# Kernel tuning notes

Hardware: AMD Instinct MI355X
Metric: run time of the kernel (lower is better)

Reference implementation:

```python
import jax, jax.numpy as jnp
import numpy as np

NUM_GRAPHS = 256
NEG_SLOPE = 0.2


def gat_layer(x, src, dst, W, a_src, a_dst, bias, concat):
    # x: [N, Fin], W: [Fin, H*C], a_src/a_dst: [H, C], bias: [H*C] or [C]
    N = x.shape[0]
    H, C = a_src.shape
    xl = (x @ W).reshape(N, H, C)                      # per-head projections
    e_src = jnp.sum(xl * a_src, axis=-1)               # [N, H]
    e_dst = jnp.sum(xl * a_dst, axis=-1)               # [N, H]
    e = jax.nn.leaky_relu(e_src[src] + e_dst[dst], NEG_SLOPE)  # [E, H]
    # edge softmax over variable-size neighbor sets (grouped by dst)
    m = jax.ops.segment_max(e, dst, num_segments=N)    # [N, H]
    m = jnp.where(jnp.isfinite(m), m, 0.0)
    ee = jnp.exp(e - m[dst])
    s = jax.ops.segment_sum(ee, dst, num_segments=N)   # [N, H]
    alpha = ee / (s[dst] + 1e-16)                      # [E, H]
    msg = alpha[:, :, None] * xl[src]                  # [E, H, C]
    out = jax.ops.segment_sum(msg, dst, num_segments=N)  # [N, H, C]
    out = out.reshape(N, H * C) if concat else out.mean(axis=1)
    return out + bias


def setup_inputs() -> dict:
    key = jax.random.key(0)
    ks = jax.random.split(key, 12)
    N, E, Fin, H, C, Fout = 100000, 1600000, 128, 8, 16, 64
    x = jax.random.normal(ks[0], (N, Fin), dtype=jnp.float32)
    edge_index = jax.random.randint(ks[1], (2, E), 0, N, dtype=jnp.int32)
    batch = jnp.sort(jax.random.randint(ks[2], (N,), 0, NUM_GRAPHS, dtype=jnp.int32))
    sc = 0.1
    W1 = jax.random.normal(ks[3], (Fin, H * C), dtype=jnp.float32) * sc
    att_src1 = jax.random.normal(ks[4], (H, C), dtype=jnp.float32) * sc
    att_dst1 = jax.random.normal(ks[5], (H, C), dtype=jnp.float32) * sc
    bias1 = jnp.zeros((H * C,), dtype=jnp.float32)
    W2 = jax.random.normal(ks[6], (H * C, Fout), dtype=jnp.float32) * sc
    att_src2 = jax.random.normal(ks[7], (1, Fout), dtype=jnp.float32) * sc
    att_dst2 = jax.random.normal(ks[8], (1, Fout), dtype=jnp.float32) * sc
    bias2 = jnp.zeros((Fout,), dtype=jnp.float32)
    return {"x": x, "W1": W1, "att_src1": att_src1, "att_dst1": att_dst1,
            "bias1": bias1, "W2": W2, "att_src2": att_src2, "att_dst2": att_dst2,
            "bias2": bias2, "edge_index": edge_index, "batch": batch}


def reference(x, W1, att_src1, att_dst1, bias1, W2, att_src2, att_dst2, bias2,
              edge_index, batch):
    N = x.shape[0]
    loop = jnp.arange(N, dtype=edge_index.dtype)
    src = jnp.concatenate([edge_index[0], loop])  # add self-loops (PyG default)
    dst = jnp.concatenate([edge_index[1], loop])
    # dropout is identity in eval mode
    h = gat_layer(x, src, dst, W1, att_src1, att_dst1, bias1, concat=True)
    h = jax.nn.elu(h)
    h = gat_layer(h, src, dst, W2, att_src2, att_dst2, bias2, concat=False)
    # global mean pooling over graphs
    sums = jax.ops.segment_sum(h, batch, num_segments=NUM_GRAPHS)
    cnts = jax.ops.segment_sum(jnp.ones((N,), h.dtype), batch, num_segments=NUM_GRAPHS)
    return sums / jnp.maximum(cnts, 1.0)[:, None]
```

## Files before the change

### kernel.cpp

```cpp
#include <hip/hip_runtime.h>
#include <hip/hip_fp16.h>


#define LRELU_SLOPE 0.2f
#define NBLKB 512
#define NBUCK 256
#define LOG2E 1.4426950408889634f

__device__ __forceinline__ float lrelu(float x) { return x > 0.f ? x : LRELU_SLOPE * x; }

typedef _Float16 f16x8 __attribute__((ext_vector_type(8)));
typedef float f32x4 __attribute__((ext_vector_type(4)));

template<typename TX, int M_, int HEADS>
__global__ __launch_bounds__(256) void gemm_mfma(const TX* __restrict__ X,
    const __half* __restrict__ Wt, __half* __restrict__ Y,
    const float* __restrict__ as, const float* __restrict__ ad,
    float* __restrict__ es, float* __restrict__ ed, int N) {
  constexpr int K = 128;
  constexpr int BM = 64;
  constexpr int LP = K + 8;
  __shared__ _Float16 Xl[BM * LP];
  const int tid = threadIdx.x;
  const int row0 = blockIdx.x * BM;

  if constexpr (sizeof(TX) == 4) {
    for (int i = tid; i < BM * (K / 4); i += 256) {
      const int r = i / (K / 4), c4 = (i % (K / 4)) * 4;
      int gr = row0 + r; if (gr >= N) gr = N - 1;
      const float4 v = *(const float4*)((const float*)X + (size_t)gr * K + c4);
      _Float16* d = &Xl[r * LP + c4];
      d[0] = (_Float16)v.x; d[1] = (_Float16)v.y;
      d[2] = (_Float16)v.z; d[3] = (_Float16)v.w;
    }
  } else {
    for (int i = tid; i < BM * (K / 8); i += 256) {
      const int r = i / (K / 8), c8 = (i % (K / 8)) * 8;
      int gr = row0 + r; if (gr >= N) gr = N - 1;
      const f16x8 v = *(const f16x8*)((const _Float16*)X + (size_t)gr * K + c8);
      *(f16x8*)&Xl[r * LP + c8] = v;
    }
  }
  __syncthreads();

  const int w = tid >> 6, l = tid & 63;
  const int lrow = l & 15, lk = (l >> 4) * 8;
  constexpr int NT = M_ / 16;
  f32x4 acc[NT];
#pragma unroll
  for (int n = 0; n < NT; ++n) acc[n] = (f32x4){0.f, 0.f, 0.f, 0.f};

#pragma unroll
  for (int kk = 0; kk < K; kk += 32) {
    const f16x8 a = *(const f16x8*)&Xl[(w * 16 + lrow) * LP + kk + lk];
#pragma unroll
    for (int n = 0; n < NT; ++n) {
      const f16x8 b = *(const f16x8*)((const _Float16*)Wt +
                        (size_t)(n * 16 + lrow) * K + kk + lk);
      acc[n] = __builtin_amdgcn_mfma_f32_16x16x32_f16(a, b, acc[n], 0, 0, 0);
    }
  }
  const int orow = row0 + w * 16 + (l >> 4) * 4;
#pragma unroll
  for (int n = 0; n < NT; ++n) {
#pragma unroll
    for (int j = 0; j < 4; ++j) {
      const int gr = orow + j;
      if (gr < N) Y[(size_t)gr * M_ + n * 16 + lrow] = __float2half(acc[n][j]);
    }
  }

  if constexpr (HEADS == 8) {
#pragma unroll
    for (int n = 0; n < NT; ++n) {
#pragma unroll
      for (int j = 0; j < 4; ++j) {
        float ps = acc[n][j] * as[n * 16 + lrow];
        float pd = acc[n][j] * ad[n * 16 + lrow];
#pragma unroll
        for (int o = 1; o <= 8; o <<= 1) {
          ps += __shfl_xor(ps, o);
          pd += __shfl_xor(pd, o);
        }
        if (lrow == n) {
          const int gr = orow + j;
          if (gr < N) { es[gr * 8 + n] = ps * LOG2E; ed[gr * 8 + n] = pd * LOG2E; }
        }
      }
    }
  } else {
#pragma unroll
    for (int j = 0; j < 4; ++j) {
      float ps = 0.f, pd = 0.f;
#pragma unroll
      for (int n = 0; n < NT; ++n) {
        ps += acc[n][j] * as[n * 16 + lrow];
        pd += acc[n][j] * ad[n * 16 + lrow];
      }
#pragma unroll
      for (int o = 1; o <= 8; o <<= 1) {
        ps += __shfl_xor(ps, o);
        pd += __shfl_xor(pd, o);
      }
      if (lrow == 0) {
        const int gr = orow + j;
        if (gr < N) { es[gr] = ps * LOG2E; ed[gr] = pd * LOG2E; }
      }
    }
  }
}

__global__ __launch_bounds__(1024) void hist_conv(const int* __restrict__ ei, int E,
    int* __restrict__ bh, const float* __restrict__ W1, const float* __restrict__ W2,
    __half* __restrict__ Wt1, __half* __restrict__ Wt2) {
  const int t = threadIdx.x;
  if (blockIdx.x < NBLKB) {
    __shared__ int hist[NBUCK];
    if (t < NBUCK) hist[t] = 0;
    __syncthreads();
    const int chunk = (E + NBLKB - 1) / NBLKB;
    const int s0 = blockIdx.x * chunk;
    const int s1 = min(E, s0 + chunk);
    for (int e = s0 + t; e < s1; e += 1024) atomicAdd(&hist[ei[E + e] >> 9], 1);
    __syncthreads();
    if (t < NBUCK) bh[t * NBLKB + blockIdx.x] = hist[t];
  } else {
    const int i = (blockIdx.x - NBLKB) * 1024 + t;
    if (i < 128 * 128) {
      const int k = i >> 7, m = i & 127;
      Wt1[m * 128 + k] = __float2half(W1[i]);
    } else if (i < 128 * 128 + 128 * 64) {
      const int j = i - 128 * 128;
      const int k = j >> 6, m = j & 63;
      Wt2[m * 128 + k] = __float2half(W2[j]);
    }
  }
}

__global__ __launch_bounds__(256) void scanA(int* __restrict__ a, int* __restrict__ ctot, int N) {
  __shared__ int sm[256];
  const int base = blockIdx.x * 1024;
  const int t = threadIdx.x;
  int v[4], s = 0;
#pragma unroll
  for (int i = 0; i < 4; ++i) {
    const int idx = base + t * 4 + i;
    v[i] = (idx < N) ? a[idx] : 0;
    s += v[i];
  }
  sm[t] = s;
  __syncthreads();
  for (int o = 1; o < 256; o <<= 1) {
    const int x = (t >= o) ? sm[t - o] : 0;
    __syncthreads();
    sm[t] += x;
    __syncthreads();
  }
  if (t == 255) ctot[blockIdx.x] = sm[255];
  int run = sm[t] - s;
#pragma unroll
  for (int i = 0; i < 4; ++i) {
    const int idx = base + t * 4 + i;
    if (idx < N) a[idx] = run;
    run += v[i];
  }
}

__global__ __launch_bounds__(256) void scanC(int* __restrict__ a,
    const int* __restrict__ ctot, int NCH, int Ntot) {
  __shared__ int sc[128];
  const int t = threadIdx.x;
  if (t < 128) sc[t] = (t < NCH) ? ctot[t] : 0;
  __syncthreads();
  for (int o = 1; o < 128; o <<= 1) {
    int x = 0;
    if (t < 128 && t >= o) x = sc[t - o];
    __syncthreads();
    if (t < 128) sc[t] += x;
    __syncthreads();
  }
  const int i = blockIdx.x * 256 + t;
  if (i < Ntot) {
    const int c = i >> 10;
    a[i] += (c == 0) ? 0 : sc[c - 1];
  }
}

__global__ __launch_bounds__(1024) void bucket_scatter(const int* __restrict__ ei, int E,
    const int* __restrict__ bh, int* __restrict__ eb) {
  __shared__ int offs[NBUCK];
  const int t = threadIdx.x;
  if (t < NBUCK) offs[t] = bh[t * NBLKB + blockIdx.x];
  __syncthreads();
  const int chunk = (E + NBLKB - 1) / NBLKB;
  const int s0 = blockIdx.x * chunk;
  const int s1 = min(E, s0 + chunk);
  for (int e = s0 + t; e < s1; e += 1024) {
    const int s = ei[e], d = ei[E + e];
    const int pos = atomicAdd(&offs[d >> 9], 1);
    eb[pos] = (s << 9) | (d & 511);
  }
}

__global__ __launch_bounds__(512) void csr_bucket(const int* __restrict__ eb,
    const int* __restrict__ bh, int E, int N,
    int* __restrict__ rowptr, int* __restrict__ csr) {
  __shared__ int deg[512];
  __shared__ int sm[512];
  const int t = threadIdx.x;
  const int bucket = blockIdx.x;
  const int bstart = bh[bucket * NBLKB];
  const int bend = (bucket + 1 < NBUCK) ? bh[(bucket + 1) * NBLKB] : E;
  const int n0 = bucket << 9;
  deg[t] = 0;
  __syncthreads();
  for (int j = bstart + t; j < bend; j += 512) atomicAdd(&deg[eb[j] & 511], 1);
  __syncthreads();
  const int v = deg[t];
  sm[t] = v;
  __syncthreads();
  for (int o = 1; o < 512; o <<= 1) {
    const int x = (t >= o) ? sm[t - o] : 0;
    __syncthreads();
    sm[t] += x;
    __syncthreads();
  }
  if (n0 + t < N) rowptr[n0 + t] = bstart + sm[t];
  deg[t] = bstart + sm[t] - v;
  __syncthreads();
  const int nband = (N + 8191) >> 13;
  for (int b = 0; b < nband; ++b) {
    for (int j = bstart + t; j < bend; j += 512) {
      const int e = eb[j];
      if ((e >> 22) == b) {
        const int pos = atomicAdd(&deg[e & 511], 1);
        csr[pos] = e >> 9;
      }
    }
  }
}

__global__ __launch_bounds__(256) void gather_h8(const __half* __restrict__ xl,
    const float* __restrict__ es, const float* __restrict__ ed,
    const int* __restrict__ rowptr, const int* __restrict__ csr,
    const float* __restrict__ bias, __half* __restrict__ hout, int N) {
  const int wave = threadIdx.x >> 6, lane = threadIdx.x & 63;
  const int n = blockIdx.x * 4 + wave;
  if (n >= N) return;
  const int sub = lane >> 5;
  const int sl  = lane & 31;
  const int c0  = sl * 4;
  const int h   = sl >> 2;
  const float edv = ed[n * 8 + h];
  const int start = (n == 0) ? 0 : rowptr[n - 1];
  const int end   = rowptr[n];
  union U8 { uint2 u; __half2 h2[2]; };

  float4 acc = make_float4(0.f, 0.f, 0.f, 0.f);
  float ssum = 0.f;
  if (sub == 0) {
    const float ee = exp2f(lrelu(es[n * 8 + h] + edv));
    U8 r; r.u = *(const uint2*)&xl[(size_t)n * 128 + c0];
    const float2 f0 = __half22float2(r.h2[0]), f1 = __half22float2(r.h2[1]);
    acc.x = ee * f0.x; acc.y = ee * f0.y; acc.z = ee * f1.x; acc.w = ee * f1.y;
    ssum = ee;
  }
  int j = start + sub;
  for (; j + 6 < end; j += 8) {
    int s0 = csr[j], s1 = csr[j + 2], s2 = csr[j + 4], s3 = csr[j + 6];
    float ev[4]; U8 r[4];
    ev[0] = es[s0 * 8 + h]; r[0].u = *(const uint2*)&xl[(size_t)s0 * 128 + c0];
    ev[1] = es[s1 * 8 + h]; r[1].u = *(const uint2*)&xl[(size_t)s1 * 128 + c0];
    ev[2] = es[s2 * 8 + h]; r[2].u = *(const uint2*)&xl[(size_t)s2 * 128 + c0];
    ev[3] = es[s3 * 8 + h]; r[3].u = *(const uint2*)&xl[(size_t)s3 * 128 + c0];
#pragma unroll
    for (int k = 0; k < 4; ++k) {
      const float ee = exp2f(lrelu(ev[k] + edv));
      const float2 f0 = __half22float2(r[k].h2[0]), f1 = __half22float2(r[k].h2[1]);
      acc.x += ee * f0.x; acc.y += ee * f0.y;
      acc.z += ee * f1.x; acc.w += ee * f1.y;
      ssum += ee;
    }
  }
  for (; j < end; j += 2) {
    const int src = csr[j];
    const float ee = exp2f(lrelu(es[src * 8 + h] + edv));
    U8 r; r.u = *(const uint2*)&xl[(size_t)src * 128 + c0];
    const float2 f0 = __half22float2(r.h2[0]), f1 = __half22float2(r.h2[1]);
    acc.x += ee * f0.x; acc.y += ee * f0.y;
    acc.z += ee * f1.x; acc.w += ee * f1.y;
    ssum += ee;
  }
  acc.x += __shfl_xor(acc.x, 32); acc.y += __shfl_xor(acc.y, 32);
  acc.z += __shfl_xor(acc.z, 32); acc.w += __shfl_xor(acc.w, 32);
  ssum  += __shfl_xor(ssum, 32);
  if (sub == 0) {
    const float inv = 1.f / (ssum + 1e-16f);
    const float4 b4 = *(const float4*)&bias[c0];
    float v0 = acc.x * inv + b4.x, v1 = acc.y * inv + b4.y;
    float v2 = acc.z * inv + b4.z, v3 = acc.w * inv + b4.w;
    v0 = v0 > 0.f ? v0 : __expf(v0) - 1.f;
    v1 = v1 > 0.f ? v1 : __expf(v1) - 1.f;
    v2 = v2 > 0.f ? v2 : __expf(v2) - 1.f;
    v3 = v3 > 0.f ? v3 : __expf(v3) - 1.f;
    U8 o; o.h2[0] = __floats2half2_rn(v0, v1); o.h2[1] = __floats2half2_rn(v2, v3);
    *(uint2*)&hout[(size_t)n * 128 + c0] = o.u;
  }
}

__global__ __launch_bounds__(256) void gather_h1(const __half* __restrict__ xl2,
    const float* __restrict__ es, const float* __restrict__ ed,
    const int* __restrict__ rowptr, const int* __restrict__ csr,
    const float* __restrict__ bias, float* __restrict__ vout, int N) {
  const int wave = threadIdx.x >> 6, lane = threadIdx.x & 63;
  const int n = blockIdx.x * 4 + wave;
  if (n >= N) return;
  const int sub = lane >> 4;
  const int sl  = lane & 15;
  const int c0  = sl * 4;
  const float edv = ed[n];
  const int start = (n == 0) ? 0 : rowptr[n - 1];
  const int end   = rowptr[n];
  union U8 { uint2 u; __half2 h2[2]; };

  float4 acc = make_float4(0.f, 0.f, 0.f, 0.f);
  float ssum = 0.f;
  if (sub == 0) {
    const float ee = exp2f(lrelu(es[n] + edv));
    U8 r; r.u = *(const uint2*)&xl2[(size_t)n * 64 + c0];
    const float2 f0 = __half22float2(r.h2[0]), f1 = __half22float2(r.h2[1]);
    acc.x = ee * f0.x; acc.y = ee * f0.y; acc.z = ee * f1.x; acc.w = ee * f1.y;
    ssum = ee;
  }
  int j = start + sub;
  for (; j + 4 < end; j += 8) {
    const int s0 = csr[j], s1 = csr[j + 4];
    const float e0 = es[s0], e1 = es[s1];
    U8 r0, r1;
    r0.u = *(const uint2*)&xl2[(size_t)s0 * 64 + c0];
    r1.u = *(const uint2*)&xl2[(size_t)s1 * 64 + c0];
    {
      const float ee = exp2f(lrelu(e0 + edv));
      const float2 f0 = __half22float2(r0.h2[0]), f1 = __half22float2(r0.h2[1]);
      acc.x += ee * f0.x; acc.y += ee * f0.y;
      acc.z += ee * f1.x; acc.w += ee * f1.y; ssum += ee;
    }
    {
      const float ee = exp2f(lrelu(e1 + edv));
      const float2 f0 = __half22float2(r1.h2[0]), f1 = __half22float2(r1.h2[1]);
      acc.x += ee * f0.x; acc.y += ee * f0.y;
      acc.z += ee * f1.x; acc.w += ee * f1.y; ssum += ee;
    }
  }
  for (; j < end; j += 4) {
    const int src = csr[j];
    const float ee = exp2f(lrelu(es[src] + edv));
    U8 r; r.u = *(const uint2*)&xl2[(size_t)src * 64 + c0];
    const float2 f0 = __half22float2(r.h2[0]), f1 = __half22float2(r.h2[1]);
    acc.x += ee * f0.x; acc.y += ee * f0.y;
    acc.z += ee * f1.x; acc.w += ee * f1.y; ssum += ee;
  }
#pragma unroll
  for (int o = 16; o <= 32; o <<= 1) {
    acc.x += __shfl_xor(acc.x, o); acc.y += __shfl_xor(acc.y, o);
    acc.z += __shfl_xor(acc.z, o); acc.w += __shfl_xor(acc.w, o);
    ssum  += __shfl_xor(ssum, o);
  }
  if (sub == 0) {
    const float inv = 1.f / (ssum + 1e-16f);
    const float4 b4 = *(const float4*)&bias[c0];
    float4 o;
    o.x = acc.x * inv + b4.x; o.y = acc.y * inv + b4.y;
    o.z = acc.z * inv + b4.z; o.w = acc.w * inv + b4.w;
    *(float4*)&vout[(size_t)n * 64 + c0] = o;
  }
}

__global__ __launch_bounds__(256) void pool_seg(const float* __restrict__ v,
    const int* __restrict__ batch, float* __restrict__ out, int N) {
  const int g = blockIdx.x;
  const int t = threadIdx.x;
  int lo = 0, hi = N;
  while (lo < hi) { const int m = (lo + hi) >> 1; if (batch[m] < g) lo = m + 1; else hi = m; }
  const int start = lo;
  hi = N;
  while (lo < hi) { const int m = (lo + hi) >> 1; if (batch[m] <= g) lo = m + 1; else hi = m; }
  const int end = lo;

  const int c = t & 63, rg = t >> 6;
  float s = 0.f;
  for (int r = start + rg; r < end; r += 4) s += v[(size_t)r * 64 + c];
  __shared__ float sm[256];
  sm[t] = s;
  __syncthreads();
  if (t < 64) {
    const float tot = sm[t] + sm[t + 64] + sm[t + 128] + sm[t + 192];
    out[g * 64 + t] = tot / fmaxf((float)(end - start), 1.f);
  }
}

extern "C" void kernel_launch(void* const* d_in, const int* in_sizes, int n_in,
                              void* d_out, int out_size, void* d_ws, size_t ws_size,
                              hipStream_t stream) {
  const float* x   = (const float*)d_in[0];
  const float* W1  = (const float*)d_in[1];
  const float* as1 = (const float*)d_in[2];
  const float* ad1 = (const float*)d_in[3];
  const float* b1  = (const float*)d_in[4];
  const float* W2  = (const float*)d_in[5];
  const float* as2 = (const float*)d_in[6];
  const float* ad2 = (const float*)d_in[7];
  const float* b2  = (const float*)d_in[8];
  const int* ei    = (const int*)d_in[9];
  const int* batch = (const int*)d_in[10];
  float* out = (float*)d_out;
  const int N = in_sizes[10];
  const int E = in_sizes[9] / 2;
  const int G = out_size / 64;
  const int BH = NBUCK * NBLKB;

  char* ws = (char*)d_ws;
  __half* xl  = (__half*)ws;
  __half* h   = (__half*)(ws + (size_t)N * 256);
  __half* xl2 = xl;
  float* vbuf = (float*)(ws + (size_t)N * 256);
  float* es1  = (float*)(ws + (size_t)N * 512);
  float* ed1  = es1 + (size_t)N * 8;
  float* es2  = es1;
  float* ed2  = es1 + N;
  int* rowptr = (int*)(ed1 + (size_t)N * 8);
  int* csr    = rowptr + N;
  int* eb     = csr + E;
  int* bh     = eb + E;
  int* ctot   = bh + BH;
  __half* Wt1 = (__half*)((((uintptr_t)(ctot + 128)) + 31) & ~(uintptr_t)31);
  __half* Wt2 = Wt1 + 128 * 128;

  hist_conv<<<NBLKB + 24, 1024, 0, stream>>>(ei, E, bh, W1, W2, Wt1, Wt2);
  scanA<<<BH / 1024, 256, 0, stream>>>(bh, ctot, BH);
  scanC<<<BH / 256, 256, 0, stream>>>(bh, ctot, BH / 1024, BH);
  bucket_scatter<<<NBLKB, 1024, 0, stream>>>(ei, E, bh, eb);
  csr_bucket<<<(N + 511) / 512, 512, 0, stream>>>(eb, bh, E, N, rowptr, csr);

  gemm_mfma<float, 128, 8><<<(N + 63) / 64, 256, 0, stream>>>(x, Wt1, xl, as1, ad1, es1, ed1, N);
  gather_h8<<<(N + 3) / 4, 256, 0, stream>>>(xl, es1, ed1, rowptr, csr, b1, h, N);

  gemm_mfma<__half, 64, 1><<<(N + 63) / 64, 256, 0, stream>>>(h, Wt2, xl2, as2, ad2, es2, ed2, N);
  gather_h1<<<(N + 3) / 4, 256, 0, stream>>>(xl2, es2, ed2, rowptr, csr, b2, vbuf, N);

  pool_seg<<<G, 256, 0, stream>>>(vbuf, batch, out, N);
}
```

Before: 320.3 us.

## Fuse CSR build with layer-1 GEMM and widen gather_h8 to 16-byte loads

Merges the CSR bucket build and the first-layer MFMA GEMM into one launch, with block ranges picking the role and shared memory shared through a union. The GEMM blocks now cover 128 rows with 512 threads. The CSR scatter drops its band-ordered multi-pass loop and scatters every edge in one pass, which cuts repeated reads of eb but loses the band locality of the csr writes. gather_h8 now has each lane handle 8 channels with 16-byte loads across 4 edge sub-streams instead of 2, and both gathers compute their two exponentials before accumulating. The layer-2 GEMM becomes a non-template specialization.

```diff
diff --git a/kernel.cpp b/kernel.cpp
--- a/kernel.cpp
+++ b/kernel.cpp
@@ -11,104 +11,6 @@
 
 typedef _Float16 f16x8 __attribute__((ext_vector_type(8)));
 typedef float f32x4 __attribute__((ext_vector_type(4)));
-
-template<typename TX, int M_, int HEADS>
-__global__ __launch_bounds__(256) void gemm_mfma(const TX* __restrict__ X,
-    const __half* __restrict__ Wt, __half* __restrict__ Y,
-    const float* __restrict__ as, const float* __restrict__ ad,
-    float* __restrict__ es, float* __restrict__ ed, int N) {
-  constexpr int K = 128;
-  constexpr int BM = 64;
-  constexpr int LP = K + 8;
-  __shared__ _Float16 Xl[BM * LP];
-  const int tid = threadIdx.x;
-  const int row0 = blockIdx.x * BM;
-
-  if constexpr (sizeof(TX) == 4) {
-    for (int i = tid; i < BM * (K / 4); i += 256) {
-      const int r = i / (K / 4), c4 = (i % (K / 4)) * 4;
-      int gr = row0 + r; if (gr >= N) gr = N - 1;
-      const float4 v = *(const float4*)((const float*)X + (size_t)gr * K + c4);
-      _Float16* d = &Xl[r * LP + c4];
-      d[0] = (_Float16)v.x; d[1] = (_Float16)v.y;
-      d[2] = (_Float16)v.z; d[3] = (_Float16)v.w;
-    }
-  } else {
-    for (int i = tid; i < BM * (K / 8); i += 256) {
-      const int r = i / (K / 8), c8 = (i % (K / 8)) * 8;
-      int gr = row0 + r; if (gr >= N) gr = N - 1;
-      const f16x8 v = *(const f16x8*)((const _Float16*)X + (size_t)gr * K + c8);
-      *(f16x8*)&Xl[r * LP + c8] = v;
-    }
-  }
-  __syncthreads();
-
-  const int w = tid >> 6, l = tid & 63;
-  const int lrow = l & 15, lk = (l >> 4) * 8;
-  constexpr int NT = M_ / 16;
-  f32x4 acc[NT];
-#pragma unroll
-  for (int n = 0; n < NT; ++n) acc[n] = (f32x4){0.f, 0.f, 0.f, 0.f};
-
-#pragma unroll
-  for (int kk = 0; kk < K; kk += 32) {
-    const f16x8 a = *(const f16x8*)&Xl[(w * 16 + lrow) * LP + kk + lk];
-#pragma unroll
-    for (int n = 0; n < NT; ++n) {
-      const f16x8 b = *(const f16x8*)((const _Float16*)Wt +
-                        (size_t)(n * 16 + lrow) * K + kk + lk);
-      acc[n] = __builtin_amdgcn_mfma_f32_16x16x32_f16(a, b, acc[n], 0, 0, 0);
-    }
-  }
-  const int orow = row0 + w * 16 + (l >> 4) * 4;
-#pragma unroll
-  for (int n = 0; n < NT; ++n) {
-#pragma unroll
-    for (int j = 0; j < 4; ++j) {
-      const int gr = orow + j;
-      if (gr < N) Y[(size_t)gr * M_ + n * 16 + lrow] = __float2half(acc[n][j]);
-    }
-  }
-
-  if constexpr (HEADS == 8) {
-#pragma unroll
-    for (int n = 0; n < NT; ++n) {
-#pragma unroll
-      for (int j = 0; j < 4; ++j) {
-        float ps = acc[n][j] * as[n * 16 + lrow];
-        float pd = acc[n][j] * ad[n * 16 + lrow];
-#pragma unroll
-        for (int o = 1; o <= 8; o <<= 1) {
-          ps += __shfl_xor(ps, o);
-          pd += __shfl_xor(pd, o);
-        }
-        if (lrow == n) {
-          const int gr = orow + j;
-          if (gr < N) { es[gr * 8 + n] = ps * LOG2E; ed[gr * 8 + n] = pd * LOG2E; }
-        }
-      }
-    }
-  } else {
-#pragma unroll
-    for (int j = 0; j < 4; ++j) {
-      float ps = 0.f, pd = 0.f;
-#pragma unroll
-      for (int n = 0; n < NT; ++n) {
-        ps += acc[n][j] * as[n * 16 + lrow];
-        pd += acc[n][j] * ad[n * 16 + lrow];
-      }
-#pragma unroll
-      for (int o = 1; o <= 8; o <<= 1) {
-        ps += __shfl_xor(ps, o);
-        pd += __shfl_xor(pd, o);
-      }
-      if (lrow == 0) {
-        const int gr = orow + j;
-        if (gr < N) { es[gr] = ps * LOG2E; ed[gr] = pd * LOG2E; }
-      }
-    }
-  }
-}
 
 __global__ __launch_bounds__(1024) void hist_conv(const int* __restrict__ ei, int E,
     int* __restrict__ bh, const float* __restrict__ W1, const float* __restrict__ W2,
@@ -202,40 +104,157 @@
   }
 }
 
-__global__ __launch_bounds__(512) void csr_bucket(const int* __restrict__ eb,
-    const int* __restrict__ bh, int E, int N,
-    int* __restrict__ rowptr, int* __restrict__ csr) {
-  __shared__ int deg[512];
-  __shared__ int sm[512];
-  const int t = threadIdx.x;
-  const int bucket = blockIdx.x;
-  const int bstart = bh[bucket * NBLKB];
-  const int bend = (bucket + 1 < NBUCK) ? bh[(bucket + 1) * NBLKB] : E;
-  const int n0 = bucket << 9;
-  deg[t] = 0;
-  __syncthreads();
-  for (int j = bstart + t; j < bend; j += 512) atomicAdd(&deg[eb[j] & 511], 1);
-  __syncthreads();
-  const int v = deg[t];
-  sm[t] = v;
-  __syncthreads();
-  for (int o = 1; o < 512; o <<= 1) {
-    const int x = (t >= o) ? sm[t - o] : 0;
-    __syncthreads();
-    sm[t] += x;
-    __syncthreads();
-  }
-  if (n0 + t < N) rowptr[n0 + t] = bstart + sm[t];
-  deg[t] = bstart + sm[t] - v;
-  __syncthreads();
-  const int nband = (N + 8191) >> 13;
-  for (int b = 0; b < nband; ++b) {
+__global__ __launch_bounds__(512) void csrb_gemm1(
+    const int* __restrict__ eb, const int* __restrict__ bh, int E,
+    int* __restrict__ rowptr, int* __restrict__ csr, int nbCsr,
+    const float* __restrict__ X, const __half* __restrict__ Wt,
+    __half* __restrict__ Y, const float* __restrict__ as,
+    const float* __restrict__ ad, float* __restrict__ es, float* __restrict__ ed,
+    int N) {
+  __shared__ union U {
+    struct { int deg[512]; int sm[512]; } c;
+    _Float16 xl[128 * 136];
+  } u;
+  const int t = threadIdx.x;
+
+  if (blockIdx.x < nbCsr) {
+    const int bucket = blockIdx.x;
+    const int bstart = bh[bucket * NBLKB];
+    const int bend = (bucket + 1 < NBUCK) ? bh[(bucket + 1) * NBLKB] : E;
+    const int n0 = bucket << 9;
+    u.c.deg[t] = 0;
+    __syncthreads();
+    for (int j = bstart + t; j < bend; j += 512) atomicAdd(&u.c.deg[eb[j] & 511], 1);
+    __syncthreads();
+    const int v = u.c.deg[t];
+    u.c.sm[t] = v;
+    __syncthreads();
+    for (int o = 1; o < 512; o <<= 1) {
+      const int x = (t >= o) ? u.c.sm[t - o] : 0;
+      __syncthreads();
+      u.c.sm[t] += x;
+      __syncthreads();
+    }
+    if (n0 + t < N) rowptr[n0 + t] = bstart + u.c.sm[t];
+    u.c.deg[t] = bstart + u.c.sm[t] - v;
+    __syncthreads();
     for (int j = bstart + t; j < bend; j += 512) {
       const int e = eb[j];
-      if ((e >> 22) == b) {
-        const int pos = atomicAdd(&deg[e & 511], 1);
-        csr[pos] = e >> 9;
+      const int pos = atomicAdd(&u.c.deg[e & 511], 1);
+      csr[pos] = e >> 9;
+    }
+  } else {
+    constexpr int K = 128, LP = 136, NT = 8;
+    const int row0 = (blockIdx.x - nbCsr) * 128;
+    for (int i = t; i < 128 * (K / 4); i += 512) {
+      const int r = i / (K / 4), c4 = (i % (K / 4)) * 4;
+      int gr = row0 + r; if (gr >= N) gr = N - 1;
+      const float4 vv = *(const float4*)(X + (size_t)gr * K + c4);
+      _Float16* d = &u.xl[r * LP + c4];
+      d[0] = (_Float16)vv.x; d[1] = (_Float16)vv.y;
+      d[2] = (_Float16)vv.z; d[3] = (_Float16)vv.w;
+    }
+    __syncthreads();
+
+    const int w = t >> 6, l = t & 63;
+    const int lrow = l & 15, lk = (l >> 4) * 8;
+    f32x4 acc[NT];
+#pragma unroll
+    for (int n = 0; n < NT; ++n) acc[n] = (f32x4){0.f, 0.f, 0.f, 0.f};
+#pragma unroll
+    for (int kk = 0; kk < K; kk += 32) {
+      const f16x8 a = *(const f16x8*)&u.xl[(w * 16 + lrow) * LP + kk + lk];
+#pragma unroll
+      for (int n = 0; n < NT; ++n) {
+        const f16x8 b = *(const f16x8*)((const _Float16*)Wt +
+                          (size_t)(n * 16 + lrow) * K + kk + lk);
+        acc[n] = __builtin_amdgcn_mfma_f32_16x16x32_f16(a, b, acc[n], 0, 0, 0);
       }
+    }
+    const int orow = row0 + w * 16 + (l >> 4) * 4;
+#pragma unroll
+    for (int n = 0; n < NT; ++n) {
+#pragma unroll
+      for (int j = 0; j < 4; ++j) {
+        const int gr = orow + j;
+        if (gr < N) Y[(size_t)gr * 128 + n * 16 + lrow] = __float2half(acc[n][j]);
+      }
+    }
+#pragma unroll
+    for (int n = 0; n < NT; ++n) {
+#pragma unroll
+      for (int j = 0; j < 4; ++j) {
+        float ps = acc[n][j] * as[n * 16 + lrow];
+        float pd = acc[n][j] * ad[n * 16 + lrow];
+#pragma unroll
+        for (int o = 1; o <= 8; o <<= 1) {
+          ps += __shfl_xor(ps, o);
+          pd += __shfl_xor(pd, o);
+        }
+        if (lrow == n) {
+          const int gr = orow + j;
+          if (gr < N) { es[gr * 8 + n] = ps * LOG2E; ed[gr * 8 + n] = pd * LOG2E; }
+        }
+      }
+    }
+  }
+}
+
+__global__ __launch_bounds__(256) void gemm2(const __half* __restrict__ X,
+    const __half* __restrict__ Wt, __half* __restrict__ Y,
+    const float* __restrict__ as, const float* __restrict__ ad,
+    float* __restrict__ es, float* __restrict__ ed, int N) {
+  constexpr int K = 128, BM = 64, LP = 136, NT = 4;
+  __shared__ _Float16 Xl[BM * LP];
+  const int tid = threadIdx.x;
+  const int row0 = blockIdx.x * BM;
+  for (int i = tid; i < BM * (K / 8); i += 256) {
+    const int r = i / (K / 8), c8 = (i % (K / 8)) * 8;
+    int gr = row0 + r; if (gr >= N) gr = N - 1;
+    const f16x8 v = *(const f16x8*)((const _Float16*)X + (size_t)gr * K + c8);
+    *(f16x8*)&Xl[r * LP + c8] = v;
+  }
+  __syncthreads();
+  const int w = tid >> 6, l = tid & 63;
+  const int lrow = l & 15, lk = (l >> 4) * 8;
+  f32x4 acc[NT];
+#pragma unroll
+  for (int n = 0; n < NT; ++n) acc[n] = (f32x4){0.f, 0.f, 0.f, 0.f};
+#pragma unroll
+  for (int kk = 0; kk < K; kk += 32) {
+    const f16x8 a = *(const f16x8*)&Xl[(w * 16 + lrow) * LP + kk + lk];
+#pragma unroll
+    for (int n = 0; n < NT; ++n) {
+      const f16x8 b = *(const f16x8*)((const _Float16*)Wt +
+                        (size_t)(n * 16 + lrow) * K + kk + lk);
+      acc[n] = __builtin_amdgcn_mfma_f32_16x16x32_f16(a, b, acc[n], 0, 0, 0);
+    }
+  }
+  const int orow = row0 + w * 16 + (l >> 4) * 4;
+#pragma unroll
+  for (int n = 0; n < NT; ++n) {
+#pragma unroll
+    for (int j = 0; j < 4; ++j) {
+      const int gr = orow + j;
+      if (gr < N) Y[(size_t)gr * 64 + n * 16 + lrow] = __float2half(acc[n][j]);
+    }
+  }
+#pragma unroll
+  for (int j = 0; j < 4; ++j) {
+    float ps = 0.f, pd = 0.f;
+#pragma unroll
+    for (int n = 0; n < NT; ++n) {
+      ps += acc[n][j] * as[n * 16 + lrow];
+      pd += acc[n][j] * ad[n * 16 + lrow];
+    }
+#pragma unroll
+    for (int o = 1; o <= 8; o <<= 1) {
+      ps += __shfl_xor(ps, o);
+      pd += __shfl_xor(pd, o);
+    }
+    if (lrow == 0) {
+      const int gr = orow + j;
+      if (gr < N) { es[gr] = ps * LOG2E; ed[gr] = pd * LOG2E; }
     }
   }
 }
@@ -247,64 +266,77 @@
   const int wave = threadIdx.x >> 6, lane = threadIdx.x & 63;
   const int n = blockIdx.x * 4 + wave;
   if (n >= N) return;
-  const int sub = lane >> 5;
-  const int sl  = lane & 31;
-  const int c0  = sl * 4;
-  const int h   = sl >> 2;
+  const int sub = lane >> 4;
+  const int sl  = lane & 15;
+  const int c0  = sl * 8;
+  const int h   = sl >> 1;
   const float edv = ed[n * 8 + h];
   const int start = (n == 0) ? 0 : rowptr[n - 1];
   const int end   = rowptr[n];
-  union U8 { uint2 u; __half2 h2[2]; };
-
-  float4 acc = make_float4(0.f, 0.f, 0.f, 0.f);
+  union U16 { uint4 u; __half2 h2[4]; };
+
+  float acc[8] = {0.f, 0.f, 0.f, 0.f, 0.f, 0.f, 0.f, 0.f};
   float ssum = 0.f;
   if (sub == 0) {
     const float ee = exp2f(lrelu(es[n * 8 + h] + edv));
-    U8 r; r.u = *(const uint2*)&xl[(size_t)n * 128 + c0];
-    const float2 f0 = __half22float2(r.h2[0]), f1 = __half22float2(r.h2[1]);
-    acc.x = ee * f0.x; acc.y = ee * f0.y; acc.z = ee * f1.x; acc.w = ee * f1.y;
+    U16 r; r.u = *(const uint4*)&xl[(size_t)n * 128 + c0];
+#pragma unroll
+    for (int q = 0; q < 4; ++q) {
+      const float2 f = __half22float2(r.h2[q]);
+      acc[2 * q] += ee * f.x; acc[2 * q + 1] += ee * f.y;
+    }
     ssum = ee;
   }
   int j = start + sub;
-  for (; j + 6 < end; j += 8) {
-    int s0 = csr[j], s1 = csr[j + 2], s2 = csr[j + 4], s3 = csr[j + 6];
-    float ev[4]; U8 r[4];
-    ev[0] = es[s0 * 8 + h]; r[0].u = *(const uint2*)&xl[(size_t)s0 * 128 + c0];
-    ev[1] = es[s1 * 8 + h]; r[1].u = *(const uint2*)&xl[(size_t)s1 * 128 + c0];
-    ev[2] = es[s2 * 8 + h]; r[2].u = *(const uint2*)&xl[(size_t)s2 * 128 + c0];
-    ev[3] = es[s3 * 8 + h]; r[3].u = *(const uint2*)&xl[(size_t)s3 * 128 + c0];
-#pragma unroll
-    for (int k = 0; k < 4; ++k) {
-      const float ee = exp2f(lrelu(ev[k] + edv));
-      const float2 f0 = __half22float2(r[k].h2[0]), f1 = __half22float2(r[k].h2[1]);
-      acc.x += ee * f0.x; acc.y += ee * f0.y;
-      acc.z += ee * f1.x; acc.w += ee * f1.y;
-      ssum += ee;
-    }
-  }
-  for (; j < end; j += 2) {
+  for (; j + 4 < end; j += 8) {
+    const int s0 = csr[j], s1 = csr[j + 4];
+    const float e0 = es[s0 * 8 + h], e1 = es[s1 * 8 + h];
+    U16 r0, r1;
+    r0.u = *(const uint4*)&xl[(size_t)s0 * 128 + c0];
+    r1.u = *(const uint4*)&xl[(size_t)s1 * 128 + c0];
+    const float ee0 = exp2f(lrelu(e0 + edv));
+    const float ee1 = exp2f(lrelu(e1 + edv));
+#pragma unroll
+    for (int q = 0; q < 4; ++q) {
+      const float2 f0 = __half22float2(r0.h2[q]);
+      const float2 f1 = __half22float2(r1.h2[q]);
+      acc[2 * q]     += ee0 * f0.x + ee1 * f1.x;
+      acc[2 * q + 1] += ee0 * f0.y + ee1 * f1.y;
+    }
+    ssum += ee0 + ee1;
+  }
+  for (; j < end; j += 4) {
     const int src = csr[j];
     const float ee = exp2f(lrelu(es[src * 8 + h] + edv));
-    U8 r; r.u = *(const uint2*)&xl[(size_t)src * 128 + c0];
-    const float2 f0 = __half22float2(r.h2[0]), f1 = __half22float2(r.h2[1]);
-    acc.x += ee * f0.x; acc.y += ee * f0.y;
-    acc.z += ee * f1.x; acc.w += ee * f1.y;
+    U16 r; r.u = *(const uint4*)&xl[(size_t)src * 128 + c0];
+#pragma unroll
+    for (int q = 0; q < 4; ++q) {
+      const float2 f = __half22float2(r.h2[q]);
+      acc[2 * q] += ee * f.x; acc[2 * q + 1] += ee * f.y;
+    }
     ssum += ee;
   }
-  acc.x += __shfl_xor(acc.x, 32); acc.y += __shfl_xor(acc.y, 32);
-  acc.z += __shfl_xor(acc.z, 32); acc.w += __shfl_xor(acc.w, 32);
-  ssum  += __shfl_xor(ssum, 32);
+#pragma unroll
+  for (int o = 16; o <= 32; o <<= 1) {
+#pragma unroll
+    for (int q = 0; q < 8; ++q) acc[q] += __shfl_xor(acc[q], o);
+    ssum += __shfl_xor(ssum, o);
+  }
   if (sub == 0) {
     const float inv = 1.f / (ssum + 1e-16f);
-    const float4 b4 = *(const float4*)&bias[c0];
-    float v0 = acc.x * inv + b4.x, v1 = acc.y * inv + b4.y;
-    float v2 = acc.z * inv + b4.z, v3 = acc.w * inv + b4.w;
-    v0 = v0 > 0.f ? v0 : __expf(v0) - 1.f;
-    v1 = v1 > 0.f ? v1 : __expf(v1) - 1.f;
-    v2 = v2 > 0.f ? v2 : __expf(v2) - 1.f;
-    v3 = v3 > 0.f ? v3 : __expf(v3) - 1.f;
-    U8 o; o.h2[0] = __floats2half2_rn(v0, v1); o.h2[1] = __floats2half2_rn(v2, v3);
-    *(uint2*)&hout[(size_t)n * 128 + c0] = o.u;
+    const float4 b0 = *(const float4*)&bias[c0];
+    const float4 b1 = *(const float4*)&bias[c0 + 4];
+    float v[8];
+    v[0] = acc[0] * inv + b0.x; v[1] = acc[1] * inv + b0.y;
+    v[2] = acc[2] * inv + b0.z; v[3] = acc[3] * inv + b0.w;
+    v[4] = acc[4] * inv + b1.x; v[5] = acc[5] * inv + b1.y;
+    v[6] = acc[6] * inv + b1.z; v[7] = acc[7] * inv + b1.w;
+#pragma unroll
+    for (int q = 0; q < 8; ++q) v[q] = v[q] > 0.f ? v[q] : __expf(v[q]) - 1.f;
+    U16 o;
+#pragma unroll
+    for (int q = 0; q < 4; ++q) o.h2[q] = __floats2half2_rn(v[2 * q], v[2 * q + 1]);
+    *(uint4*)&hout[(size_t)n * 128 + c0] = o.u;
   }
 }
 
@@ -339,18 +371,19 @@
     U8 r0, r1;
     r0.u = *(const uint2*)&xl2[(size_t)s0 * 64 + c0];
     r1.u = *(const uint2*)&xl2[(size_t)s1 * 64 + c0];
+    const float ee0 = exp2f(lrelu(e0 + edv));
+    const float ee1 = exp2f(lrelu(e1 + edv));
     {
-      const float ee = exp2f(lrelu(e0 + edv));
       const float2 f0 = __half22float2(r0.h2[0]), f1 = __half22float2(r0.h2[1]);
-      acc.x += ee * f0.x; acc.y += ee * f0.y;
-      acc.z += ee * f1.x; acc.w += ee * f1.y; ssum += ee;
+      acc.x += ee0 * f0.x; acc.y += ee0 * f0.y;
+      acc.z += ee0 * f1.x; acc.w += ee0 * f1.y;
     }
     {
-      const float ee = exp2f(lrelu(e1 + edv));
       const float2 f0 = __half22float2(r1.h2[0]), f1 = __half22float2(r1.h2[1]);
-      acc.x += ee * f0.x; acc.y += ee * f0.y;
-      acc.z += ee * f1.x; acc.w += ee * f1.y; ssum += ee;
-    }
+      acc.x += ee1 * f0.x; acc.y += ee1 * f0.y;
+      acc.z += ee1 * f1.x; acc.w += ee1 * f1.y;
+    }
+    ssum += ee0 + ee1;
   }
   for (; j < end; j += 4) {
     const int src = csr[j];
@@ -418,6 +451,8 @@
   const int E = in_sizes[9] / 2;
   const int G = out_size / 64;
   const int BH = NBUCK * NBLKB;
+  const int nbCsr = (N + 511) / 512;
+  const int nbGemm1 = (N + 127) / 128;
 
   char* ws = (char*)d_ws;
   __half* xl  = (__half*)ws;
@@ -440,12 +475,12 @@
   scanA<<<BH / 1024, 256, 0, stream>>>(bh, ctot, BH);
   scanC<<<BH / 256, 256, 0, stream>>>(bh, ctot, BH / 1024, BH);
   bucket_scatter<<<NBLKB, 1024, 0, stream>>>(ei, E, bh, eb);
-  csr_bucket<<<(N + 511) / 512, 512, 0, stream>>>(eb, bh, E, N, rowptr, csr);
-
-  gemm_mfma<float, 128, 8><<<(N + 63) / 64, 256, 0, stream>>>(x, Wt1, xl, as1, ad1, es1, ed1, N);
+
+  csrb_gemm1<<<nbCsr + nbGemm1, 512, 0, stream>>>(eb, bh, E, rowptr, csr, nbCsr,
+      x, Wt1, xl, as1, ad1, es1, ed1, N);
   gather_h8<<<(N + 3) / 4, 256, 0, stream>>>(xl, es1, ed1, rowptr, csr, b1, h, N);
 
-  gemm_mfma<__half, 64, 1><<<(N + 63) / 64, 256, 0, stream>>>(h, Wt2, xl2, as2, ad2, es2, ed2, N);
+  gemm2<<<(N + 63) / 64, 256, 0, stream>>>(h, Wt2, xl2, as2, ad2, es2, ed2, N);
   gather_h1<<<(N + 3) / 4, 256, 0, stream>>>(xl2, es2, ed2, rowptr, csr, b2, vbuf, N);
 
   pool_seg<<<G, 256, 0, stream>>>(vbuf, batch, out, N);
```

Result: faster. 269.5 us (-15.9%).
